# Optimization experiments

Hardware: AMD Instinct MI355X
Metric: run time of the kernel (lower is better)

Reference implementation:

```python
import jax, jax.numpy as jnp
import numpy as np

B, N, F, FE, H, C = 2, 2048, 128, 8, 4, 64
LEAKY_ALPHA = 0.2
NEG_INF = -1e9


def setup_inputs() -> dict:
    key = jax.random.key(0)
    ks = jax.random.split(key, 8)
    return {
        "X": jax.random.normal(ks[0], (B, N, F), jnp.float32),
        "A": jax.random.uniform(ks[1], (B, N, N), jnp.float32),
        "E": jax.random.normal(ks[2], (B, N, N, FE), jnp.float32),
        "W_edge": jax.random.normal(ks[3], (FE, 1), jnp.float32) * 0.1,
        "b_edge": jnp.zeros((1,), jnp.float32),
        "W_gat": jax.random.normal(ks[4], (H, F, C), jnp.float32) * 0.05,
        "a_src": jax.random.normal(ks[5], (H, C), jnp.float32) * 0.1,
        "a_dst": jax.random.normal(ks[6], (H, C), jnp.float32) * 0.1,
        "b_gat": jnp.zeros((H * C,), jnp.float32),
        "ln_gamma": jnp.ones((H * C,), jnp.float32),
        "ln_beta": jnp.zeros((H * C,), jnp.float32),
    }


def reference(X, A, E, W_edge, b_edge, W_gat, a_src, a_dst, b_gat, ln_gamma, ln_beta):
    # --- edge gate: sigmoid(Dense_1(E)) -> [B,N,N], multiply into adjacency ---
    edge_w = jax.nn.sigmoid(jnp.einsum("bije,eo->bijo", E, W_edge) + b_edge)
    A = A * edge_w[..., 0]  # [B,N,N]

    # --- multi-head dense GAT (spektral GATConv, concat_heads, elu) ---
    h = jnp.einsum("bnf,hfc->bnhc", X, W_gat)  # [B,N,H,C]
    s_src = jnp.einsum("bnhc,hc->bnh", h, a_src)  # [B,N,H]
    s_dst = jnp.einsum("bnhc,hc->bnh", h, a_dst)
    # e_ij = LeakyReLU(src_i + dst_j): [B,N(i),N(j),H]
    logits = jax.nn.leaky_relu(s_src[:, :, None, :] + s_dst[:, None, :, :],
                               negative_slope=LEAKY_ALPHA)
    mask = jnp.where(A == 0.0, NEG_INF, 0.0)[..., None]  # [B,N,N,1]
    attn = jax.nn.softmax(logits + mask, axis=2)  # softmax over neighbors j
    out = jnp.einsum("bijh,bjhc->bihc", attn, h)  # [B,N,H,C]
    out = out.reshape(B, N, H * C) + b_gat
    out = jax.nn.elu(out)

    # --- LayerNorm over the feature axis (inference: dropout is identity) ---
    mu = jnp.mean(out, axis=-1, keepdims=True)
    var = jnp.var(out, axis=-1, keepdims=True)
    out = (out - mu) * jax.lax.rsqrt(var + 1e-3) * ln_gamma + ln_beta
    return out
```

## Files before the change

kernel.cpp:

```cpp
#include <hip/hip_runtime.h>
#include <string.h>


#define BB 2
#define NN 2048
#define FF 128
#define HH 4
#define CC 64
#define HC 256
#define TN 8
#define ITILE 32
#define TI 8
#define LOG2E 1.4426950408889634f

typedef __attribute__((ext_vector_type(8))) short short8;
typedef __attribute__((ext_vector_type(4))) float f32x4;

__device__ __forceinline__ float wave_sum(float v) {
#pragma unroll
    for (int m = 32; m >= 1; m >>= 1) v += __shfl_xor(v, m, 64);
    return v;
}

__device__ __forceinline__ unsigned short bf16rne(float x) {
    unsigned u = __float_as_uint(x);
    return (unsigned short)((u + 0x7fffu + ((u >> 16) & 1u)) >> 16);
}

__global__ __launch_bounds__(256) void k1_proj(
    const float* __restrict__ X, const float* __restrict__ Wg,
    const float* __restrict__ a_src, const float* __restrict__ a_dst,
    unsigned short* __restrict__ hT, float* __restrict__ ssT,
    float* __restrict__ sdT)
{
    __shared__ float sX[TN][FF];
    const int blk = blockIdx.x;
    const int b  = blk / (NN / TN);
    const int n0 = (blk % (NN / TN)) * TN;
    const int tid = threadIdx.x;
    const int h = tid >> 6, c = tid & 63;

    for (int idx = tid; idx < TN * FF; idx += 256) {
        int r = idx >> 7, f = idx & 127;
        sX[r][f] = X[(size_t)(b * NN + n0 + r) * FF + f];
    }
    __syncthreads();

    float hv[TN];
#pragma unroll
    for (int r = 0; r < TN; ++r) hv[r] = 0.f;

#pragma unroll 4
    for (int f4 = 0; f4 < FF / 4; ++f4) {
        const int f = f4 * 4;
        const float w0 = Wg[(h * FF + f + 0) * CC + c];
        const float w1 = Wg[(h * FF + f + 1) * CC + c];
        const float w2 = Wg[(h * FF + f + 2) * CC + c];
        const float w3 = Wg[(h * FF + f + 3) * CC + c];
#pragma unroll
        for (int r = 0; r < TN; ++r) {
            float4 x4 = *(const float4*)&sX[r][f];
            hv[r] = fmaf(x4.x, w0, hv[r]);
            hv[r] = fmaf(x4.y, w1, hv[r]);
            hv[r] = fmaf(x4.z, w2, hv[r]);
            hv[r] = fmaf(x4.w, w3, hv[r]);
        }
    }

    union { short8 v; unsigned short u[8]; } pk;
#pragma unroll
    for (int r = 0; r < TN; ++r) pk.u[r] = bf16rne(hv[r]);
    *(short8*)&hT[((size_t)(b * HH + h) * CC + c) * NN + n0] = pk.v;

    const float as = a_src[tid];
    const float ad = a_dst[tid];
#pragma unroll
    for (int r = 0; r < TN; ++r) {
        const int n = n0 + r;
        float s1 = wave_sum(hv[r] * as);
        float s2 = wave_sum(hv[r] * ad);
        if (c == 0) {
            ssT[(b * HH + h) * NN + n] = s1 * LOG2E;
            sdT[(b * HH + h) * NN + n] = s2 * LOG2E;
        }
    }
}

__device__ __forceinline__ short8 make_p(float ss, const float4& sda, const float4& sdb,
                                         const float4& aa, const float4& ab, float& lsum)
{
    const float sd[8] = {sda.x, sda.y, sda.z, sda.w, sdb.x, sdb.y, sdb.z, sdb.w};
    const float av[8] = {aa.x, aa.y, aa.z, aa.w, ab.x, ab.y, ab.z, ab.w};
    union { short8 v; unsigned short u[8]; } pk;
#pragma unroll
    for (int t = 0; t < 8; ++t) {
        float x = ss + sd[t];
        x = fmaxf(x, 0.2f * x);
        float p = (av[t] == 0.f) ? 0.f : __builtin_amdgcn_exp2f(x);
        lsum += p;
        pk.u[t] = bf16rne(p);
    }
    return pk.v;
}

__global__ __launch_bounds__(256) void k2_attn(
    const float* __restrict__ Adj, const unsigned short* __restrict__ hT,
    const float* __restrict__ ssT, const float* __restrict__ sdT,
    float* __restrict__ pacc, float* __restrict__ plsum,
    int jparts, int jspan)
{
    const int blk  = blockIdx.x;
    const int part = blk % jparts;
    const int t2   = blk / jparts;
    const int it   = t2 % (NN / ITILE);
    const int b    = t2 / (NN / ITILE);
    const int i0   = it * ITILE;
    const int j0   = part * jspan;

    const int tid = threadIdx.x;
    const int h = tid >> 6, l = tid & 63;
    const int lr = l & 15;
    const int lq = l >> 4;

    const float ss0 = ssT[(b * HH + h) * NN + i0 + lr];
    const float ss1 = ssT[(b * HH + h) * NN + i0 + 16 + lr];

    f32x4 acc[2][4];
#pragma unroll
    for (int mi = 0; mi < 2; ++mi)
#pragma unroll
        for (int ni = 0; ni < 4; ++ni) acc[mi][ni] = (f32x4){0.f, 0.f, 0.f, 0.f};
    float lsum0 = 0.f, lsum1 = 0.f;

    const float* adj0 = Adj + (size_t)(b * NN + i0 + lr) * NN + j0 + lq * 8;
    const float* adj1 = adj0 + (size_t)16 * NN;
    const float* sdp  = sdT + (b * HH + h) * NN + j0 + lq * 8;
    const unsigned short* hb[4];
#pragma unroll
    for (int ni = 0; ni < 4; ++ni)
        hb[ni] = hT + ((size_t)(b * HH + h) * CC + ni * 16 + lr) * NN + j0 + lq * 8;

    for (int js = 0; js < jspan; js += 32) {
        const float4 a0a = *(const float4*)(adj0 + js);
        const float4 a0b = *(const float4*)(adj0 + js + 4);
        const float4 a1a = *(const float4*)(adj1 + js);
        const float4 a1b = *(const float4*)(adj1 + js + 4);
        const float4 sda = *(const float4*)(sdp + js);
        const float4 sdb = *(const float4*)(sdp + js + 4);
        short8 bfr[4];
#pragma unroll
        for (int ni = 0; ni < 4; ++ni) bfr[ni] = *(const short8*)(hb[ni] + js);

        const short8 pa0 = make_p(ss0, sda, sdb, a0a, a0b, lsum0);
        const short8 pa1 = make_p(ss1, sda, sdb, a1a, a1b, lsum1);

#pragma unroll
        for (int ni = 0; ni < 4; ++ni) {
            acc[0][ni] = __builtin_amdgcn_mfma_f32_16x16x32_bf16(pa0, bfr[ni], acc[0][ni], 0, 0, 0);
            acc[1][ni] = __builtin_amdgcn_mfma_f32_16x16x32_bf16(pa1, bfr[ni], acc[1][ni], 0, 0, 0);
        }
    }

    lsum0 += __shfl_xor(lsum0, 16, 64); lsum0 += __shfl_xor(lsum0, 32, 64);
    lsum1 += __shfl_xor(lsum1, 16, 64); lsum1 += __shfl_xor(lsum1, 32, 64);
    if (lq == 0) {
        plsum[((size_t)(part * BB + b) * HH + h) * NN + i0 + lr]      = lsum0;
        plsum[((size_t)(part * BB + b) * HH + h) * NN + i0 + 16 + lr] = lsum1;
    }

#pragma unroll
    for (int mi = 0; mi < 2; ++mi)
#pragma unroll
        for (int ni = 0; ni < 4; ++ni)
#pragma unroll
            for (int r = 0; r < 4; ++r) {
                const int i  = i0 + mi * 16 + lq * 4 + r;
                const int hc = h * 64 + ni * 16 + lr;
                pacc[((size_t)(part * BB + b) * NN + i) * HC + hc] = acc[mi][ni][r];
            }
}

__global__ __launch_bounds__(256) void k3_epi(
    const float* __restrict__ pacc, const float* __restrict__ plsum,
    const float* __restrict__ b_gat, const float* __restrict__ gamma,
    const float* __restrict__ beta, float* __restrict__ out, int jparts)
{
    __shared__ float red1[HH][TI], red2[HH][TI];
    const int blk = blockIdx.x;
    const int b  = blk / (NN / TI);
    const int i0 = (blk % (NN / TI)) * TI;
    const int tid = threadIdx.x;
    const int h = tid >> 6, lane = tid & 63;

    float vals[TI];
    const float bg = b_gat[tid];
#pragma unroll
    for (int ti = 0; ti < TI; ++ti) {
        const int i = i0 + ti;
        float a = 0.f, l = 0.f;
        for (int part = 0; part < jparts; ++part) {
            a += pacc[((size_t)(part * BB + b) * NN + i) * HC + tid];
            l += plsum[((size_t)(part * BB + b) * HH + h) * NN + i];
        }
        float v = a / l + bg;
        v = (v > 0.f) ? v : (__expf(v) - 1.f);
        vals[ti] = v;
        float s1 = wave_sum(v);
        float s2 = wave_sum(v * v);
        if (lane == 0) { red1[h][ti] = s1; red2[h][ti] = s2; }
    }
    __syncthreads();

    const float g = gamma[tid], bt = beta[tid];
#pragma unroll
    for (int ti = 0; ti < TI; ++ti) {
        float s1 = red1[0][ti] + red1[1][ti] + red1[2][ti] + red1[3][ti];
        float s2 = red2[0][ti] + red2[1][ti] + red2[2][ti] + red2[3][ti];
        float mu  = s1 * (1.f / HC);
        float var = s2 * (1.f / HC) - mu * mu;
        float inv = rsqrtf(var + 1e-3f);
        out[(size_t)(b * NN + i0 + ti) * HC + tid] = (vals[ti] - mu) * inv * g + bt;
    }
}

extern "C" void kernel_launch(void* const* d_in, const int* in_sizes, int n_in,
                              void* d_out, int out_size, void* d_ws, size_t ws_size,
                              hipStream_t stream)
{
    const float* X     = (const float*)d_in[0];
    const float* Adj   = (const float*)d_in[1];
    const float* Wg    = (const float*)d_in[5];
    const float* a_src = (const float*)d_in[6];
    const float* a_dst = (const float*)d_in[7];
    const float* b_gat = (const float*)d_in[8];
    const float* gam   = (const float*)d_in[9];
    const float* bet   = (const float*)d_in[10];
    float* out = (float*)d_out;

    const size_t hT_elems   = (size_t)BB * HH * CC * NN;
    const size_t ss_elems   = (size_t)BB * HH * NN;
    const size_t lsum_part  = (size_t)BB * HH * NN;
    const size_t pacc_part  = (size_t)BB * NN * HC;

    unsigned short* hT = (unsigned short*)d_ws;
    float* ssT   = (float*)(hT + hT_elems);
    float* sdT   = ssT + ss_elems;
    float* plsum = sdT + ss_elems;

    const size_t fixed_bytes = hT_elems * 2 + ss_elems * 8;
    int jparts = 4;
    while (jparts > 1 &&
           fixed_bytes + (size_t)jparts * (lsum_part + pacc_part) * 4 > ws_size)
        jparts >>= 1;
    float* pacc = plsum + (size_t)jparts * lsum_part;
    const int jspan = NN / jparts;

    k1_proj<<<BB * NN / TN, 256, 0, stream>>>(X, Wg, a_src, a_dst, hT, ssT, sdT);
    k2_attn<<<BB * (NN / ITILE) * jparts, 256, 0, stream>>>(
        Adj, hT, ssT, sdT, pacc, plsum, jparts, jspan);
    k3_epi<<<BB * NN / TI, 256, 0, stream>>>(pacc, plsum, b_gat, gam, bet, out, jparts);
}
```

Baseline: 389.1 us.

## Fuse split-j reduction and LayerNorm epilogue into attention kernel via LDS

Removes the separate epilogue kernel and the global partial-accumulator buffers. Each block now handles 16 rows with 8 waves (4 heads × 2 j-halves). The halves are combined through shared memory, and the normalize, bias, ELU and LayerNorm steps run in the same kernel. The bf16 packing is switched to the paired conversion intrinsic. In exchange, each block now covers fewer rows, so reuse of the hT tiles drops, and the grid has fewer, larger blocks.

```diff
diff --git a/kernel.cpp b/kernel.cpp
--- a/kernel.cpp
+++ b/kernel.cpp
@@ -1,5 +1,5 @@
 #include <hip/hip_runtime.h>
-#include <string.h>
+#include <hip/hip_bf16.h>
 
 
 #define BB 2
@@ -9,8 +9,6 @@
 #define CC 64
 #define HC 256
 #define TN 8
-#define ITILE 32
-#define TI 8
 #define LOG2E 1.4426950408889634f
 
 typedef __attribute__((ext_vector_type(8))) short short8;
@@ -91,135 +89,148 @@
 {
     const float sd[8] = {sda.x, sda.y, sda.z, sda.w, sdb.x, sdb.y, sdb.z, sdb.w};
     const float av[8] = {aa.x, aa.y, aa.z, aa.w, ab.x, ab.y, ab.z, ab.w};
-    union { short8 v; unsigned short u[8]; } pk;
+    float p[8];
 #pragma unroll
     for (int t = 0; t < 8; ++t) {
         float x = ss + sd[t];
         x = fmaxf(x, 0.2f * x);
-        float p = (av[t] == 0.f) ? 0.f : __builtin_amdgcn_exp2f(x);
-        lsum += p;
-        pk.u[t] = bf16rne(p);
-    }
+        float pv = (av[t] == 0.f) ? 0.f : __builtin_amdgcn_exp2f(x);
+        lsum += pv;
+        p[t] = pv;
+    }
+    union { short8 v; __hip_bfloat162 h2[4]; } pk;
+#pragma unroll
+    for (int t = 0; t < 4; ++t)
+        pk.h2[t] = __float22bfloat162_rn(make_float2(p[2 * t], p[2 * t + 1]));
     return pk.v;
 }
 
-__global__ __launch_bounds__(256) void k2_attn(
+__global__ __launch_bounds__(512) void k2_attn(
     const float* __restrict__ Adj, const unsigned short* __restrict__ hT,
     const float* __restrict__ ssT, const float* __restrict__ sdT,
-    float* __restrict__ pacc, float* __restrict__ plsum,
-    int jparts, int jspan)
-{
-    const int blk  = blockIdx.x;
-    const int part = blk % jparts;
-    const int t2   = blk / jparts;
-    const int it   = t2 % (NN / ITILE);
-    const int b    = t2 / (NN / ITILE);
-    const int i0   = it * ITILE;
-    const int j0   = part * jspan;
-
-    const int tid = threadIdx.x;
-    const int h = tid >> 6, l = tid & 63;
+    const float* __restrict__ b_gat, const float* __restrict__ gamma,
+    const float* __restrict__ beta, float* __restrict__ out)
+{
+    __shared__ float accs[16][HH][64];
+    __shared__ float lsumx[HH][16];
+    __shared__ float red1s[HH][16], red2s[HH][16];
+
+    const int blk = blockIdx.x;
+    const int b  = blk >> 7;
+    const int i0 = (blk & 127) << 4;
+    const int tid  = threadIdx.x;
+    const int wave = tid >> 6;
+    const int h  = wave & 3;
+    const int jh = wave >> 2;
+    const int l  = tid & 63;
     const int lr = l & 15;
     const int lq = l >> 4;
 
-    const float ss0 = ssT[(b * HH + h) * NN + i0 + lr];
-    const float ss1 = ssT[(b * HH + h) * NN + i0 + 16 + lr];
-
-    f32x4 acc[2][4];
-#pragma unroll
-    for (int mi = 0; mi < 2; ++mi)
-#pragma unroll
-        for (int ni = 0; ni < 4; ++ni) acc[mi][ni] = (f32x4){0.f, 0.f, 0.f, 0.f};
-    float lsum0 = 0.f, lsum1 = 0.f;
-
-    const float* adj0 = Adj + (size_t)(b * NN + i0 + lr) * NN + j0 + lq * 8;
-    const float* adj1 = adj0 + (size_t)16 * NN;
-    const float* sdp  = sdT + (b * HH + h) * NN + j0 + lq * 8;
+    const float ss = ssT[(b * HH + h) * NN + i0 + lr];
+
+    f32x4 acc[4];
+#pragma unroll
+    for (int ni = 0; ni < 4; ++ni) acc[ni] = (f32x4){0.f, 0.f, 0.f, 0.f};
+    float lsum = 0.f;
+
+    const float* adjp = Adj + (size_t)(b * NN + i0 + lr) * NN + jh * 1024 + lq * 8;
+    const float* sdp  = sdT + (b * HH + h) * NN + jh * 1024 + lq * 8;
     const unsigned short* hb[4];
 #pragma unroll
     for (int ni = 0; ni < 4; ++ni)
-        hb[ni] = hT + ((size_t)(b * HH + h) * CC + ni * 16 + lr) * NN + j0 + lq * 8;
-
-    for (int js = 0; js < jspan; js += 32) {
-        const float4 a0a = *(const float4*)(adj0 + js);
-        const float4 a0b = *(const float4*)(adj0 + js + 4);
-        const float4 a1a = *(const float4*)(adj1 + js);
-        const float4 a1b = *(const float4*)(adj1 + js + 4);
+        hb[ni] = hT + ((size_t)(b * HH + h) * CC + ni * 16 + lr) * NN + jh * 1024 + lq * 8;
+
+    for (int js = 0; js < 1024; js += 32) {
+        const float4 aa  = *(const float4*)(adjp + js);
+        const float4 ab  = *(const float4*)(adjp + js + 4);
         const float4 sda = *(const float4*)(sdp + js);
         const float4 sdb = *(const float4*)(sdp + js + 4);
         short8 bfr[4];
 #pragma unroll
         for (int ni = 0; ni < 4; ++ni) bfr[ni] = *(const short8*)(hb[ni] + js);
 
-        const short8 pa0 = make_p(ss0, sda, sdb, a0a, a0b, lsum0);
-        const short8 pa1 = make_p(ss1, sda, sdb, a1a, a1b, lsum1);
-
-#pragma unroll
-        for (int ni = 0; ni < 4; ++ni) {
-            acc[0][ni] = __builtin_amdgcn_mfma_f32_16x16x32_bf16(pa0, bfr[ni], acc[0][ni], 0, 0, 0);
-            acc[1][ni] = __builtin_amdgcn_mfma_f32_16x16x32_bf16(pa1, bfr[ni], acc[1][ni], 0, 0, 0);
-        }
-    }
-
-    lsum0 += __shfl_xor(lsum0, 16, 64); lsum0 += __shfl_xor(lsum0, 32, 64);
-    lsum1 += __shfl_xor(lsum1, 16, 64); lsum1 += __shfl_xor(lsum1, 32, 64);
-    if (lq == 0) {
-        plsum[((size_t)(part * BB + b) * HH + h) * NN + i0 + lr]      = lsum0;
-        plsum[((size_t)(part * BB + b) * HH + h) * NN + i0 + 16 + lr] = lsum1;
-    }
-
-#pragma unroll
-    for (int mi = 0; mi < 2; ++mi)
+        const short8 pa = make_p(ss, sda, sdb, aa, ab, lsum);
 #pragma unroll
         for (int ni = 0; ni < 4; ++ni)
+            acc[ni] = __builtin_amdgcn_mfma_f32_16x16x32_bf16(pa, bfr[ni], acc[ni], 0, 0, 0);
+    }
+
+    lsum += __shfl_xor(lsum, 16, 64);
+    lsum += __shfl_xor(lsum, 32, 64);
+
+    if (jh == 1) {
+        if (lq == 0) lsumx[h][lr] = lsum;
+#pragma unroll
+        for (int ni = 0; ni < 4; ++ni)
+#pragma unroll
+            for (int r = 0; r < 4; ++r)
+                accs[ni * 4 + r][h][l] = acc[ni][r];
+    }
+    __syncthreads();
+
+    float vals[4][4];
+    float s1[4], s2[4];
+    if (jh == 0) {
+        const float lcomb = lsum + lsumx[h][lr];
+        float lrow[4];
+#pragma unroll
+        for (int r = 0; r < 4; ++r) lrow[r] = __shfl(lcomb, lq * 4 + r, 64);
+
+        float bg[4];
+#pragma unroll
+        for (int ni = 0; ni < 4; ++ni) bg[ni] = b_gat[h * 64 + ni * 16 + lr];
+
+#pragma unroll
+        for (int r = 0; r < 4; ++r) { s1[r] = 0.f; s2[r] = 0.f; }
+#pragma unroll
+        for (int ni = 0; ni < 4; ++ni)
 #pragma unroll
             for (int r = 0; r < 4; ++r) {
-                const int i  = i0 + mi * 16 + lq * 4 + r;
-                const int hc = h * 64 + ni * 16 + lr;
-                pacc[((size_t)(part * BB + b) * NN + i) * HC + hc] = acc[mi][ni][r];
+                float a = acc[ni][r] + accs[ni * 4 + r][h][l];
+                float v = a / lrow[r] + bg[ni];
+                v = (v > 0.f) ? v : (__expf(v) - 1.f);
+                vals[ni][r] = v;
+                s1[r] += v;
+                s2[r] += v * v;
             }
-}
-
-__global__ __launch_bounds__(256) void k3_epi(
-    const float* __restrict__ pacc, const float* __restrict__ plsum,
-    const float* __restrict__ b_gat, const float* __restrict__ gamma,
-    const float* __restrict__ beta, float* __restrict__ out, int jparts)
-{
-    __shared__ float red1[HH][TI], red2[HH][TI];
-    const int blk = blockIdx.x;
-    const int b  = blk / (NN / TI);
-    const int i0 = (blk % (NN / TI)) * TI;
-    const int tid = threadIdx.x;
-    const int h = tid >> 6, lane = tid & 63;
-
-    float vals[TI];
-    const float bg = b_gat[tid];
-#pragma unroll
-    for (int ti = 0; ti < TI; ++ti) {
-        const int i = i0 + ti;
-        float a = 0.f, l = 0.f;
-        for (int part = 0; part < jparts; ++part) {
-            a += pacc[((size_t)(part * BB + b) * NN + i) * HC + tid];
-            l += plsum[((size_t)(part * BB + b) * HH + h) * NN + i];
-        }
-        float v = a / l + bg;
-        v = (v > 0.f) ? v : (__expf(v) - 1.f);
-        vals[ti] = v;
-        float s1 = wave_sum(v);
-        float s2 = wave_sum(v * v);
-        if (lane == 0) { red1[h][ti] = s1; red2[h][ti] = s2; }
+#pragma unroll
+        for (int m = 1; m <= 8; m <<= 1) {
+#pragma unroll
+            for (int r = 0; r < 4; ++r) {
+                s1[r] += __shfl_xor(s1[r], m, 64);
+                s2[r] += __shfl_xor(s2[r], m, 64);
+            }
+        }
+        if (lr == 0) {
+#pragma unroll
+            for (int r = 0; r < 4; ++r) {
+                red1s[h][lq * 4 + r] = s1[r];
+                red2s[h][lq * 4 + r] = s2[r];
+            }
+        }
     }
     __syncthreads();
 
-    const float g = gamma[tid], bt = beta[tid];
-#pragma unroll
-    for (int ti = 0; ti < TI; ++ti) {
-        float s1 = red1[0][ti] + red1[1][ti] + red1[2][ti] + red1[3][ti];
-        float s2 = red2[0][ti] + red2[1][ti] + red2[2][ti] + red2[3][ti];
-        float mu  = s1 * (1.f / HC);
-        float var = s2 * (1.f / HC) - mu * mu;
-        float inv = rsqrtf(var + 1e-3f);
-        out[(size_t)(b * NN + i0 + ti) * HC + tid] = (vals[ti] - mu) * inv * g + bt;
+    if (jh == 0) {
+        const float g = gamma[h * 64 + lr], g1 = gamma[h * 64 + 16 + lr],
+                    g2 = gamma[h * 64 + 32 + lr], g3 = gamma[h * 64 + 48 + lr];
+        const float bt = beta[h * 64 + lr], bt1 = beta[h * 64 + 16 + lr],
+                    bt2 = beta[h * 64 + 32 + lr], bt3 = beta[h * 64 + 48 + lr];
+        const float gm[4] = {g, g1, g2, g3};
+        const float bm[4] = {bt, bt1, bt2, bt3};
+#pragma unroll
+        for (int r = 0; r < 4; ++r) {
+            const int row = lq * 4 + r;
+            float S1 = red1s[0][row] + red1s[1][row] + red1s[2][row] + red1s[3][row];
+            float S2 = red2s[0][row] + red2s[1][row] + red2s[2][row] + red2s[3][row];
+            float mu  = S1 * (1.f / HC);
+            float var = S2 * (1.f / HC) - mu * mu;
+            float inv = rsqrtf(var + 1e-3f);
+            float* op = out + (size_t)(b * NN + i0 + row) * HC + h * 64 + lr;
+#pragma unroll
+            for (int ni = 0; ni < 4; ++ni)
+                op[ni * 16] = (vals[ni][r] - mu) * inv * gm[ni] + bm[ni];
+        }
     }
 }
 
@@ -237,26 +248,13 @@
     const float* bet   = (const float*)d_in[10];
     float* out = (float*)d_out;
 
-    const size_t hT_elems   = (size_t)BB * HH * CC * NN;
-    const size_t ss_elems   = (size_t)BB * HH * NN;
-    const size_t lsum_part  = (size_t)BB * HH * NN;
-    const size_t pacc_part  = (size_t)BB * NN * HC;
+    const size_t hT_elems = (size_t)BB * HH * CC * NN;
+    const size_t ss_elems = (size_t)BB * HH * NN;
 
     unsigned short* hT = (unsigned short*)d_ws;
-    float* ssT   = (float*)(hT + hT_elems);
-    float* sdT   = ssT + ss_elems;
-    float* plsum = sdT + ss_elems;
-
-    const size_t fixed_bytes = hT_elems * 2 + ss_elems * 8;
-    int jparts = 4;
-    while (jparts > 1 &&
-           fixed_bytes + (size_t)jparts * (lsum_part + pacc_part) * 4 > ws_size)
-        jparts >>= 1;
-    float* pacc = plsum + (size_t)jparts * lsum_part;
-    const int jspan = NN / jparts;
+    float* ssT = (float*)(hT + hT_elems);
+    float* sdT = ssT + ss_elems;
 
     k1_proj<<<BB * NN / TN, 256, 0, stream>>>(X, Wg, a_src, a_dst, hT, ssT, sdT);
-    k2_attn<<<BB * (NN / ITILE) * jparts, 256, 0, stream>>>(
-        Adj, hT, ssT, sdT, pacc, plsum, jparts, jspan);
-    k3_epi<<<BB * NN / TI, 256, 0, stream>>>(pacc, plsum, b_gat, gam, bet, out, jparts);
-}
+    k2_attn<<<BB * (NN / 16), 512, 0, stream>>>(Adj, hT, ssT, sdT, b_gat, gam, bet, out);
+}
```

Result: no change. 389.9 us (+0.2%).
